# Performance work log

Measured on AMD Instinct MI355X. Metric: run time of the kernel, lower is better.

Reference implementation:

```python
import jax, jax.numpy as jnp
import numpy as np

B, T, D, H = 4, 2048, 1024, 16
HD = D // H  # head_dim = 64
SCALE = HD ** -0.5


def setup_inputs() -> dict:
    key = jax.random.key(0)
    k1, k2, k3 = jax.random.split(key, 3)
    x = jax.random.normal(k1, (B, T, D), dtype=jnp.float32)
    # xavier-uniform-like scaling for weights
    qkv_w = jax.random.normal(k2, (3 * D, D), dtype=jnp.float32) * (2.0 / (4 * D)) ** 0.5
    out_w = jax.random.normal(k3, (D, D), dtype=jnp.float32) * (1.0 / D) ** 0.5
    out_b = jnp.zeros((D,), dtype=jnp.float32)
    return {"x": x, "qkv_w": qkv_w, "out_w": out_w, "out_b": out_b}


def reference(x, qkv_w, out_w, out_b):
    Bx, Tx, _ = x.shape
    # qkv projection (nn.Linear: x @ W^T), no bias
    qkv = jnp.einsum('btd,ed->bte', x, qkv_w)  # [B,T,3D]
    qkv = qkv.reshape(Bx, Tx, 3, H, HD).transpose(2, 0, 3, 1, 4)  # [3,B,H,T,hd]
    q, k, v = qkv[0], qkv[1], qkv[2]
    scores = jnp.einsum('bhqd,bhkd->bhqk', q, k) * SCALE  # [B,H,T,T]
    causal = jnp.triu(jnp.ones((Tx, Tx), dtype=bool), k=1)
    scores = jnp.where(causal, -jnp.inf, scores)
    weights = jax.nn.softmax(scores, axis=-1)
    out = jnp.einsum('bhqk,bhkd->bhqd', weights, v)  # [B,H,T,hd]
    out = out.transpose(0, 2, 1, 3).reshape(Bx, Tx, D)
    return jnp.einsum('btd,ed->bte', out, out_w) + out_b
```

## Files before the change

### kernel.cpp

```cpp
#include <hip/hip_runtime.h>
#include <stdint.h>


typedef __bf16 bfx8 __attribute__((ext_vector_type(8)));
typedef float f32x4 __attribute__((ext_vector_type(4)));
typedef float f32x16 __attribute__((ext_vector_type(16)));

__device__ __forceinline__ uint16_t f2b(float f) {
  uint32_t u = __float_as_uint(f);
  u += 0x7fff + ((u >> 16) & 1);
  return (uint16_t)(u >> 16);
}

__device__ __forceinline__ uint32_t cvt_pk(float lo, float hi) {
  uint32_t r;
  asm("v_cvt_pk_bf16_f32 %0, %1, %2" : "=v"(r) : "v"(lo), "v"(hi));
  return r;
}

__device__ __forceinline__ void gld16(const void* g, void* l) {
  __builtin_amdgcn_global_load_lds((const __attribute__((address_space(1))) void*)g,
                                   (__attribute__((address_space(3))) void*)l,
                                   16, 0, 0);
}

__global__ __launch_bounds__(256) void cvt_all(const float* __restrict__ x,
                                               const float* __restrict__ w1,
                                               const float* __restrict__ w2,
                                               uint16_t* __restrict__ xb,
                                               uint16_t* __restrict__ w1b,
                                               uint16_t* __restrict__ w2b) {
  int i = blockIdx.x * 256 + threadIdx.x;
  const float* in;
  uint16_t* out;
  if (i < 1048576) { in = x; out = xb; }
  else if (i < 1048576 + 393216) { in = w1; out = w1b; i -= 1048576; }
  else { in = w2; out = w2b; i -= 1048576 + 393216; }
  float4 a = ((const float4*)in)[2 * i];
  float4 b = ((const float4*)in)[2 * i + 1];
  union { uint16_t u[8]; uint4 v; } pk;
  pk.u[0] = f2b(a.x); pk.u[1] = f2b(a.y); pk.u[2] = f2b(a.z); pk.u[3] = f2b(a.w);
  pk.u[4] = f2b(b.x); pk.u[5] = f2b(b.y); pk.u[6] = f2b(b.z); pk.u[7] = f2b(b.w);
  ((uint4*)out)[i] = pk.v;
}

template <int NI, int OUTF32, int QSC>
__global__ __launch_bounds__(512, 2) void gemm8p(const uint16_t* __restrict__ A,
                                                 const uint16_t* __restrict__ B,
                                                 void* __restrict__ Cout,
                                                 const float* __restrict__ bias,
                                                 int M, int N, int K, int nbx, int nwg) {
  constexpr int G0 = (NI + 1) / 2;
  constexpr int G1 = NI - G0;
  __shared__ alignas(16) uint16_t As[2][256 * 64];
  __shared__ alignas(16) uint16_t Bs[2][64 * NI * 64];

  int did = blockIdx.x;
  int wg = (did & 7) * (nwg >> 3) + (did >> 3);
  int bx = wg % nbx, by = wg / nbx;
  int m0 = by * 256, n0 = bx * (64 * NI);

  int tid = threadIdx.x, lane = tid & 63, wid = tid >> 6;
  int wm = wid >> 2, wn = wid & 3;
  int l15 = lane & 15;
  int ko = (lane >> 4) * 8;
  int sw = (l15 & 7) * 8;

  int srow = lane >> 3;
  int scol = ((lane & 7) ^ srow) * 8;

  f32x4 acc[8][NI] = {};

  auto stageA = [&](int buf, int t) {
    int k0 = t * 64;
#pragma unroll
    for (int i = 0; i < 4; ++i) {
      int r = wid * 32 + i * 8;
      gld16(&A[(size_t)(m0 + r + srow) * K + k0 + scol], &As[buf][r * 64]);
    }
  };
  auto stageB = [&](int buf, int t) {
    int k0 = t * 64;
#pragma unroll
    for (int i = 0; i < NI; ++i) {
      int r = wid * 8 * NI + i * 8;
      gld16(&B[(size_t)(n0 + r + srow) * K + k0 + scol], &Bs[buf][r * 64]);
    }
  };
  auto waitSteady = [&]() {
    if constexpr (NI == 3) asm volatile("s_waitcnt vmcnt(7)" ::: "memory");
    else                   asm volatile("s_waitcnt vmcnt(6)" ::: "memory");
  };

  stageA(0, 0); stageB(0, 0);
  stageA(1, 1); stageB(1, 1);
  waitSteady();
  __builtin_amdgcn_s_barrier();
  __builtin_amdgcn_sched_barrier(0);

  int nt = K >> 6;
  for (int t = 0; t < nt; ++t) {
    int buf = t & 1;
    const uint16_t* ap = &As[buf][0];
    const uint16_t* bp = &Bs[buf][0];
    bfx8 a[4][2], bg0[G0][2], bg1[G1][2], a2[4][2];

#pragma unroll
    for (int mi = 0; mi < 4; ++mi)
#pragma unroll
      for (int kk = 0; kk < 2; ++kk) {
        int r = wm * 128 + mi * 16 + l15;
        a[mi][kk] = *(const bfx8*)&ap[r * 64 + ((kk * 32 + ko) ^ sw)];
      }
#pragma unroll
    for (int ni = 0; ni < G0; ++ni)
#pragma unroll
      for (int kk = 0; kk < 2; ++kk) {
        int r = wn * (NI * 16) + ni * 16 + l15;
        bg0[ni][kk] = *(const bfx8*)&bp[r * 64 + ((kk * 32 + ko) ^ sw)];
      }
    __builtin_amdgcn_s_barrier();
    __builtin_amdgcn_s_setprio(1);
#pragma unroll
    for (int mi = 0; mi < 4; ++mi)
#pragma unroll
      for (int ni = 0; ni < G0; ++ni)
#pragma unroll
        for (int kk = 0; kk < 2; ++kk)
          acc[mi][ni] = __builtin_amdgcn_mfma_f32_16x16x32_bf16(a[mi][kk], bg0[ni][kk],
                                                                acc[mi][ni], 0, 0, 0);
    __builtin_amdgcn_s_setprio(0);
    __builtin_amdgcn_s_barrier();

#pragma unroll
    for (int ni = 0; ni < G1; ++ni)
#pragma unroll
      for (int kk = 0; kk < 2; ++kk) {
        int r = wn * (NI * 16) + (G0 + ni) * 16 + l15;
        bg1[ni][kk] = *(const bfx8*)&bp[r * 64 + ((kk * 32 + ko) ^ sw)];
      }
    __builtin_amdgcn_s_barrier();
    __builtin_amdgcn_s_setprio(1);
#pragma unroll
    for (int mi = 0; mi < 4; ++mi)
#pragma unroll
      for (int ni = 0; ni < G1; ++ni)
#pragma unroll
        for (int kk = 0; kk < 2; ++kk)
          acc[mi][G0 + ni] = __builtin_amdgcn_mfma_f32_16x16x32_bf16(a[mi][kk], bg1[ni][kk],
                                                                     acc[mi][G0 + ni], 0, 0, 0);
    __builtin_amdgcn_s_setprio(0);
    __builtin_amdgcn_s_barrier();

#pragma unroll
    for (int mi = 0; mi < 4; ++mi)
#pragma unroll
      for (int kk = 0; kk < 2; ++kk) {
        int r = wm * 128 + (mi + 4) * 16 + l15;
        a2[mi][kk] = *(const bfx8*)&ap[r * 64 + ((kk * 32 + ko) ^ sw)];
      }
    if (t + 2 < nt) stageB(buf, t + 2);
    __builtin_amdgcn_s_barrier();
    __builtin_amdgcn_s_setprio(1);
#pragma unroll
    for (int mi = 0; mi < 4; ++mi)
#pragma unroll
      for (int ni = 0; ni < G0; ++ni)
#pragma unroll
        for (int kk = 0; kk < 2; ++kk)
          acc[mi + 4][ni] = __builtin_amdgcn_mfma_f32_16x16x32_bf16(a2[mi][kk], bg0[ni][kk],
                                                                    acc[mi + 4][ni], 0, 0, 0);
    __builtin_amdgcn_s_setprio(0);
    __builtin_amdgcn_s_barrier();

    if (t + 2 < nt) {
      stageA(buf, t + 2);
      waitSteady();
    } else if (t + 2 == nt) {
      asm volatile("s_waitcnt vmcnt(0)" ::: "memory");
    }
    __builtin_amdgcn_sched_barrier(0);
    __builtin_amdgcn_s_barrier();
    __builtin_amdgcn_s_setprio(1);
#pragma unroll
    for (int mi = 0; mi < 4; ++mi)
#pragma unroll
      for (int ni = 0; ni < G1; ++ni)
#pragma unroll
        for (int kk = 0; kk < 2; ++kk)
          acc[mi + 4][G0 + ni] = __builtin_amdgcn_mfma_f32_16x16x32_bf16(a2[mi][kk], bg1[ni][kk],
                                                                         acc[mi + 4][G0 + ni], 0, 0, 0);
    __builtin_amdgcn_s_setprio(0);
    __builtin_amdgcn_s_barrier();
  }

#pragma unroll
  for (int mi = 0; mi < 8; ++mi) {
    int row = m0 + wm * 128 + mi * 16 + ((lane >> 4) << 2);
#pragma unroll
    for (int ni = 0; ni < NI; ++ni) {
      int col = n0 + wn * (NI * 16) + ni * 16 + l15;
      float qsc = (QSC && col < 1024) ? 0.18033688f : 1.0f;
#pragma unroll
      for (int r = 0; r < 4; ++r) {
        float v = acc[mi][ni][r];
        if (OUTF32)
          ((float*)Cout)[(size_t)(row + r) * N + col] = v + bias[col];
        else
          ((uint16_t*)Cout)[(size_t)(row + r) * N + col] = f2b(v * qsc);
      }
    }
  }
}

__global__ __launch_bounds__(256, 2) void flash_attn(const uint16_t* __restrict__ qkv,
                                                     uint16_t* __restrict__ attnb) {
  const int T = 2048, D3 = 3072;
  __shared__ alignas(16) uint16_t Ks[3][64 * 64];
  __shared__ alignas(16) uint16_t Vt[3][64 * 64];

  int d = blockIdx.x;
  int bh = d & 63;
  int a = d >> 6;
  int b = bh >> 4, h = bh & 15;

  int tid = threadIdx.x, lane = tid & 63, wid = tid >> 6;
  int l31 = lane & 31, hi = lane >> 5;
  int swz = (lane & 7) << 3;

  size_t base = (size_t)b * T * D3;
  int hoff = h * 64;
  const uint16_t* kbase = &qkv[base + 1024 + hoff];
  const uint16_t* vbase = &qkv[base + 2048 + hoff];

  int krow = wid * 16 + (lane >> 3);
  int kc = ((lane & 7) << 3) ^ ((krow & 7) << 3);
  int vr = (tid & 31) * 2;
  int vc = (tid >> 5) * 8;

  for (int p = 0; p < 2; ++p) {
    int qb = (p == 0) ? (15 - a) : a;
    int q0 = qb << 7;
    int qw = q0 + wid * 32;
    int ntile = 2 * qb + 2;

    float l_r = 0.f;
    f32x16 acc0 = {}, acc1 = {};
    bfx8 pf[4];
    int smax_prev = -1, vb_prev = 0;

    bfx8 qf[4];
    {
      const uint16_t* qp = &qkv[base + (size_t)(qw + l31) * D3 + hoff + 8 * hi];
#pragma unroll
      for (int h4 = 0; h4 < 4; ++h4) qf[h4] = *(const bfx8*)(qp + 16 * h4);
    }

    uint4 vA0, vA1, vB0, vB1;

    auto loadV = [&](int kv0, uint4& r0, uint4& r1) {
      r0 = *(const uint4*)&vbase[(size_t)(kv0 + vr) * D3 + vc];
      r1 = *(const uint4*)&vbase[(size_t)(kv0 + vr + 1) * D3 + vc];
    };
    auto stageK = [&](int buf, int kv0) {
      gld16(&kbase[(size_t)(kv0 + krow) * D3 + kc], &Ks[buf][wid * 1024]);
      gld16(&kbase[(size_t)(kv0 + krow + 8) * D3 + kc], &Ks[buf][wid * 1024 + 512]);
    };
    auto writeV = [&](int vb, const uint4& r0, const uint4& r1) {
      union { uint4 v; uint16_t u[8]; } x, y;
      x.v = r0; y.v = r1;
#pragma unroll
      for (int jj = 0; jj < 8; ++jj) {
        int hd = vc + jj;
        uint32_t pk = (uint32_t)x.u[jj] | ((uint32_t)y.u[jj] << 16);
        *(uint32_t*)&Vt[vb][hd * 64 + (vr ^ ((hd & 7) << 3))] = pk;
      }
    };
    auto doPV = [&]() {
      const uint16_t* vp = &Vt[vb_prev][0];
      __builtin_amdgcn_s_setprio(1);
#pragma unroll
      for (int s = 0; s < 4; ++s) {
        if (s <= smax_prev) {
          bfx8 v0 = *(const bfx8*)&vp[l31 * 64 + ((16 * s + 8 * hi) ^ swz)];
          acc0 = __builtin_amdgcn_mfma_f32_32x32x16_bf16(v0, pf[s], acc0, 0, 0, 0);
          bfx8 v1 = *(const bfx8*)&vp[(32 + l31) * 64 + ((16 * s + 8 * hi) ^ swz)];
          acc1 = __builtin_amdgcn_mfma_f32_32x32x16_bf16(v1, pf[s], acc1, 0, 0, 0);
        }
      }
      __builtin_amdgcn_s_setprio(0);
    };

    loadV(0, vA0, vA1);
    stageK(0, 0);
    writeV(0, vA0, vA1);
    loadV(64, vB0, vB1);
    stageK(1, 64);
    asm volatile("s_waitcnt vmcnt(0) lgkmcnt(0)" ::: "memory");
    __builtin_amdgcn_s_barrier();
    __builtin_amdgcn_sched_barrier(0);

    auto subiter = [&](int t, uint4& f0, uint4& f1, uint4& c0, uint4& c1) {
      int kv0 = t << 6;
      bool issue = (t + 2 < ntile);
      if (issue) {
        loadV((t + 2) << 6, f0, f1);
        stageK((t + 2) % 3, (t + 2) << 6);
      }
      bool active = (kv0 <= qw);
      int tmax = (qw > kv0) ? 2 : 1;
      f32x16 st0 = {}, st1 = {};
      if (active) {
        const uint16_t* kp = &Ks[t % 3][0];
        __builtin_amdgcn_s_setprio(1);
#pragma unroll
        for (int h4 = 0; h4 < 4; ++h4) {
          bfx8 kf0 = *(const bfx8*)&kp[l31 * 64 + ((16 * h4 + 8 * hi) ^ swz)];
          st0 = __builtin_amdgcn_mfma_f32_32x32x16_bf16(kf0, qf[h4], st0, 0, 0, 0);
          if (tmax == 2) {
            bfx8 kf1 = *(const bfx8*)&kp[(32 + l31) * 64 + ((16 * h4 + 8 * hi) ^ swz)];
            st1 = __builtin_amdgcn_mfma_f32_32x32x16_bf16(kf1, qf[h4], st1, 0, 0, 0);
          }
        }
        __builtin_amdgcn_s_setprio(0);
      }

      if (smax_prev >= 0) { doPV(); smax_prev = -1; }

      if (active) {
        int q = qw + l31;
        if (kv0 == qw) {
#pragma unroll
          for (int r = 0; r < 16; ++r) {
            int kv = kv0 + (r & 3) + 8 * (r >> 2) + 4 * hi;
            if (kv > q) st0[r] = -1e30f;
          }
        }
        if (tmax == 2 && kv0 + 32 == qw) {
#pragma unroll
          for (int r = 0; r < 16; ++r) {
            int kv = kv0 + 32 + (r & 3) + 8 * (r >> 2) + 4 * hi;
            if (kv > q) st1[r] = -1e30f;
          }
        }
        float l0 = 0.f, l1 = 0.f, l2 = 0.f, l3 = 0.f;
#pragma unroll
        for (int r = 0; r < 16; r += 4) {
          float e0 = __builtin_amdgcn_exp2f(st0[r]);
          float e1 = __builtin_amdgcn_exp2f(st0[r + 1]);
          float e2 = __builtin_amdgcn_exp2f(st0[r + 2]);
          float e3 = __builtin_amdgcn_exp2f(st0[r + 3]);
          st0[r] = e0; st0[r + 1] = e1; st0[r + 2] = e2; st0[r + 3] = e3;
          l0 += e0; l1 += e1; l2 += e2; l3 += e3;
        }
        if (tmax == 2) {
#pragma unroll
          for (int r = 0; r < 16; r += 4) {
            float e0 = __builtin_amdgcn_exp2f(st1[r]);
            float e1 = __builtin_amdgcn_exp2f(st1[r + 1]);
            float e2 = __builtin_amdgcn_exp2f(st1[r + 2]);
            float e3 = __builtin_amdgcn_exp2f(st1[r + 3]);
            st1[r] = e0; st1[r + 1] = e1; st1[r + 2] = e2; st1[r + 3] = e3;
            l0 += e0; l1 += e1; l2 += e2; l3 += e3;
          }
        }
        l_r += (l0 + l1) + (l2 + l3);

        int smax = (qw + 31 - kv0) >> 4;
        if (smax > 3) smax = 3;
#pragma unroll
        for (int s = 0; s < 4; ++s) {
          if (s <= smax) {
            int pb = 8 * (s & 1);
            uint32_t W0, W1, W2, W3;
            if (s < 2) {
              W0 = cvt_pk(st0[pb + 0], st0[pb + 1]);
              W1 = cvt_pk(st0[pb + 2], st0[pb + 3]);
              W2 = cvt_pk(st0[pb + 4], st0[pb + 5]);
              W3 = cvt_pk(st0[pb + 6], st0[pb + 7]);
            } else {
              W0 = cvt_pk(st1[pb + 0], st1[pb + 1]);
              W1 = cvt_pk(st1[pb + 2], st1[pb + 3]);
              W2 = cvt_pk(st1[pb + 4], st1[pb + 5]);
              W3 = cvt_pk(st1[pb + 6], st1[pb + 7]);
            }
            auto rA = __builtin_amdgcn_permlane32_swap(W0, W2, false, false);
            auto rB = __builtin_amdgcn_permlane32_swap(W1, W3, false, false);
            union { uint32_t u[4]; bfx8 v; } pk;
            pk.u[0] = rA[0]; pk.u[1] = rB[0]; pk.u[2] = rA[1]; pk.u[3] = rB[1];
            pf[s] = pk.v;
          }
        }
        smax_prev = smax;
        vb_prev = t % 3;
      }

      if (t + 1 < ntile) writeV((t + 1) % 3, c0, c1);

      if (issue)
        asm volatile("s_waitcnt vmcnt(4) lgkmcnt(0)" ::: "memory");
      else
        asm volatile("s_waitcnt vmcnt(0) lgkmcnt(0)" ::: "memory");
      __builtin_amdgcn_s_barrier();
      __builtin_amdgcn_sched_barrier(0);
    };

    for (int t = 0; t < ntile; t += 2) {
      subiter(t, vA0, vA1, vB0, vB1);
      subiter(t + 1, vB0, vB1, vA0, vA1);
    }
    if (smax_prev >= 0) doPV();

    float l_tot = l_r + __shfl_xor(l_r, 32);
    __syncthreads();
    uint16_t* ow = ((uint16_t*)Ks) + wid * 2048;
    float rl = 1.0f / l_tot;
#pragma unroll
    for (int f = 0; f < 2; ++f) {
#pragma unroll
      for (int r = 0; r < 16; r += 2) {
        int hd = 32 * f + (r & 3) + 8 * (r >> 2) + 4 * hi;
        float v0 = (f ? acc1[r] : acc0[r]) * rl;
        float v1 = (f ? acc1[r + 1] : acc0[r + 1]) * rl;
        *(uint32_t*)&ow[l31 * 64 + (hd ^ ((l31 & 7) << 3))] = cvt_pk(v0, v1);
      }
    }
    int row = lane >> 1, cb = (lane & 1) * 32;
    int q = q0 + wid * 32 + row;
    int rs = (row & 7) << 3;
    uint16_t* dst = &attnb[(size_t)(b * T + q) * 1024 + hoff + cb];
#pragma unroll
    for (int cc = 0; cc < 4; ++cc)
      *(uint4*)&dst[cc * 8] = *(const uint4*)&ow[row * 64 + ((cb + cc * 8) ^ rs)];
    __syncthreads();
  }
}

extern "C" void kernel_launch(void* const* d_in, const int* in_sizes, int n_in,
                              void* d_out, int out_size, void* d_ws, size_t ws_size,
                              hipStream_t stream) {
  const float* x = (const float*)d_in[0];
  const float* qkv_w = (const float*)d_in[1];
  const float* out_w = (const float*)d_in[2];
  const float* out_b = (const float*)d_in[3];
  float* out = (float*)d_out;

  char* ws = (char*)d_ws;
  uint16_t* xb    = (uint16_t*)(ws);
  uint16_t* qkvb  = (uint16_t*)(ws + 16777216);
  uint16_t* attnb = (uint16_t*)(ws + 67108864);
  uint16_t* wqkvb = (uint16_t*)(ws + 83886080);
  uint16_t* wob   = (uint16_t*)(ws + 90177536);

  cvt_all<<<6144, 256, 0, stream>>>(x, qkv_w, out_w, xb, wqkvb, wob);

  gemm8p<3, 0, 1><<<512, 512, 0, stream>>>(xb, wqkvb, (void*)qkvb, nullptr,
                                           8192, 3072, 1024, 16, 512);
  flash_attn<<<512, 256, 0, stream>>>(qkvb, attnb);
  gemm8p<2, 1, 0><<<256, 512, 0, stream>>>(attnb, wob, (void*)out, out_b,
                                           8192, 1024, 1024, 8, 256);
}
```

Baseline: 178.4 us.

## Widen flash-attention KV tile to 128 rows with double-buffered K

The flash attention loop now processes 128 KV rows per iteration instead of 64. That halves the iteration count and barriers and gives four 32-wide score tiles per step, with K double-buffered and V triple-buffered at the larger size. Global loads are now prefetched one tile ahead instead of two, and every iteration waits on vmcnt(0). This costs more LDS and registers (pf[8], st[4]) and exposes more load latency. It may also reduce occupancy and latency hiding.

Result: slower. 182.8 us (+2.4%).

```diff
diff --git a/kernel.cpp b/kernel.cpp
--- a/kernel.cpp
+++ b/kernel.cpp
@@ -216,8 +216,8 @@
 __global__ __launch_bounds__(256, 2) void flash_attn(const uint16_t* __restrict__ qkv,
                                                      uint16_t* __restrict__ attnb) {
   const int T = 2048, D3 = 3072;
-  __shared__ alignas(16) uint16_t Ks[3][64 * 64];
-  __shared__ alignas(16) uint16_t Vt[3][64 * 64];
+  __shared__ alignas(16) uint16_t Ks[2][128 * 64];
+  __shared__ alignas(16) uint16_t Vt[3][64 * 128];
 
   int d = blockIdx.x;
   int bh = d & 63;
@@ -233,20 +233,20 @@
   const uint16_t* kbase = &qkv[base + 1024 + hoff];
   const uint16_t* vbase = &qkv[base + 2048 + hoff];
 
-  int krow = wid * 16 + (lane >> 3);
-  int kc = ((lane & 7) << 3) ^ ((krow & 7) << 3);
-  int vr = (tid & 31) * 2;
+  int ksub = lane >> 3;
+  int kc = ((lane & 7) << 3) ^ (ksub << 3);
+  int vr4 = (tid & 31) * 4;
   int vc = (tid >> 5) * 8;
 
   for (int p = 0; p < 2; ++p) {
     int qb = (p == 0) ? (15 - a) : a;
     int q0 = qb << 7;
     int qw = q0 + wid * 32;
-    int ntile = 2 * qb + 2;
+    int ntile = qb + 1;
 
     float l_r = 0.f;
     f32x16 acc0 = {}, acc1 = {};
-    bfx8 pf[4];
+    bfx8 pf[8];
     int smax_prev = -1, vb_prev = 0;
 
     bfx8 qf[4];
@@ -256,70 +256,80 @@
       for (int h4 = 0; h4 < 4; ++h4) qf[h4] = *(const bfx8*)(qp + 16 * h4);
     }
 
-    uint4 vA0, vA1, vB0, vB1;
-
-    auto loadV = [&](int kv0, uint4& r0, uint4& r1) {
-      r0 = *(const uint4*)&vbase[(size_t)(kv0 + vr) * D3 + vc];
-      r1 = *(const uint4*)&vbase[(size_t)(kv0 + vr + 1) * D3 + vc];
+    uint4 v0r, v1r, v2r, v3r;
+
+    auto loadV = [&](int kv0) {
+      const uint16_t* vp = &vbase[(size_t)(kv0 + vr4) * D3 + vc];
+      v0r = *(const uint4*)vp;
+      v1r = *(const uint4*)(vp + D3);
+      v2r = *(const uint4*)(vp + 2 * D3);
+      v3r = *(const uint4*)(vp + 3 * D3);
     };
     auto stageK = [&](int buf, int kv0) {
-      gld16(&kbase[(size_t)(kv0 + krow) * D3 + kc], &Ks[buf][wid * 1024]);
-      gld16(&kbase[(size_t)(kv0 + krow + 8) * D3 + kc], &Ks[buf][wid * 1024 + 512]);
+#pragma unroll
+      for (int i = 0; i < 4; ++i) {
+        int r = wid * 32 + i * 8;
+        gld16(&kbase[(size_t)(kv0 + r + ksub) * D3 + kc], &Ks[buf][r * 64]);
+      }
     };
-    auto writeV = [&](int vb, const uint4& r0, const uint4& r1) {
-      union { uint4 v; uint16_t u[8]; } x, y;
-      x.v = r0; y.v = r1;
-#pragma unroll
-      for (int jj = 0; jj < 8; ++jj) {
-        int hd = vc + jj;
-        uint32_t pk = (uint32_t)x.u[jj] | ((uint32_t)y.u[jj] << 16);
-        *(uint32_t*)&Vt[vb][hd * 64 + (vr ^ ((hd & 7) << 3))] = pk;
+    auto writeV = [&](int vb) {
+      union { uint4 v; uint16_t u[8]; } x0, x1, x2, x3;
+      x0.v = v0r; x1.v = v1r; x2.v = v2r; x3.v = v3r;
+#pragma unroll
+      for (int j = 0; j < 8; ++j) {
+        int hd = vc + j;
+        uint2 val;
+        val.x = (uint32_t)x0.u[j] | ((uint32_t)x1.u[j] << 16);
+        val.y = (uint32_t)x2.u[j] | ((uint32_t)x3.u[j] << 16);
+        *(uint2*)&Vt[vb][hd * 128 + (vr4 ^ ((hd & 7) << 3))] = val;
       }
     };
     auto doPV = [&]() {
       const uint16_t* vp = &Vt[vb_prev][0];
       __builtin_amdgcn_s_setprio(1);
 #pragma unroll
-      for (int s = 0; s < 4; ++s) {
+      for (int s = 0; s < 8; ++s) {
         if (s <= smax_prev) {
-          bfx8 v0 = *(const bfx8*)&vp[l31 * 64 + ((16 * s + 8 * hi) ^ swz)];
-          acc0 = __builtin_amdgcn_mfma_f32_32x32x16_bf16(v0, pf[s], acc0, 0, 0, 0);
-          bfx8 v1 = *(const bfx8*)&vp[(32 + l31) * 64 + ((16 * s + 8 * hi) ^ swz)];
-          acc1 = __builtin_amdgcn_mfma_f32_32x32x16_bf16(v1, pf[s], acc1, 0, 0, 0);
+          bfx8 va = *(const bfx8*)&vp[l31 * 128 + ((16 * s + 8 * hi) ^ swz)];
+          acc0 = __builtin_amdgcn_mfma_f32_32x32x16_bf16(va, pf[s], acc0, 0, 0, 0);
+          bfx8 vb2 = *(const bfx8*)&vp[(32 + l31) * 128 + ((16 * s + 8 * hi) ^ swz)];
+          acc1 = __builtin_amdgcn_mfma_f32_32x32x16_bf16(vb2, pf[s], acc1, 0, 0, 0);
         }
       }
       __builtin_amdgcn_s_setprio(0);
     };
 
-    loadV(0, vA0, vA1);
+    loadV(0);
     stageK(0, 0);
-    writeV(0, vA0, vA1);
-    loadV(64, vB0, vB1);
-    stageK(1, 64);
+    writeV(0);
     asm volatile("s_waitcnt vmcnt(0) lgkmcnt(0)" ::: "memory");
     __builtin_amdgcn_s_barrier();
     __builtin_amdgcn_sched_barrier(0);
 
-    auto subiter = [&](int t, uint4& f0, uint4& f1, uint4& c0, uint4& c1) {
-      int kv0 = t << 6;
-      bool issue = (t + 2 < ntile);
+    for (int t = 0; t < ntile; ++t) {
+      int kv0 = t << 7;
+      bool issue = (t + 1 < ntile);
       if (issue) {
-        loadV((t + 2) << 6, f0, f1);
-        stageK((t + 2) % 3, (t + 2) << 6);
+        loadV((t + 1) << 7);
+        stageK((t + 1) & 1, (t + 1) << 7);
       }
       bool active = (kv0 <= qw);
-      int tmax = (qw > kv0) ? 2 : 1;
-      f32x16 st0 = {}, st1 = {};
+      int dq = qw - kv0;
+      int tmax = 4, sd = -1;
+      if (active && dq < 128) { tmax = (dq >> 5) + 1; sd = dq >> 5; }
+      f32x16 st[4] = {};
+
       if (active) {
-        const uint16_t* kp = &Ks[t % 3][0];
+        const uint16_t* kp = &Ks[t & 1][0];
         __builtin_amdgcn_s_setprio(1);
 #pragma unroll
         for (int h4 = 0; h4 < 4; ++h4) {
-          bfx8 kf0 = *(const bfx8*)&kp[l31 * 64 + ((16 * h4 + 8 * hi) ^ swz)];
-          st0 = __builtin_amdgcn_mfma_f32_32x32x16_bf16(kf0, qf[h4], st0, 0, 0, 0);
-          if (tmax == 2) {
-            bfx8 kf1 = *(const bfx8*)&kp[(32 + l31) * 64 + ((16 * h4 + 8 * hi) ^ swz)];
-            st1 = __builtin_amdgcn_mfma_f32_32x32x16_bf16(kf1, qf[h4], st1, 0, 0, 0);
+#pragma unroll
+          for (int s = 0; s < 4; ++s) {
+            if (s < tmax) {
+              bfx8 kf = *(const bfx8*)&kp[(32 * s + l31) * 64 + ((16 * h4 + 8 * hi) ^ swz)];
+              st[s] = __builtin_amdgcn_mfma_f32_32x32x16_bf16(kf, qf[h4], st[s], 0, 0, 0);
+            }
           }
         }
         __builtin_amdgcn_s_setprio(0);
@@ -329,85 +339,60 @@
 
       if (active) {
         int q = qw + l31;
-        if (kv0 == qw) {
-#pragma unroll
-          for (int r = 0; r < 16; ++r) {
-            int kv = kv0 + (r & 3) + 8 * (r >> 2) + 4 * hi;
-            if (kv > q) st0[r] = -1e30f;
-          }
-        }
-        if (tmax == 2 && kv0 + 32 == qw) {
-#pragma unroll
-          for (int r = 0; r < 16; ++r) {
-            int kv = kv0 + 32 + (r & 3) + 8 * (r >> 2) + 4 * hi;
-            if (kv > q) st1[r] = -1e30f;
+#pragma unroll
+        for (int s = 0; s < 4; ++s) {
+          if (s == sd) {
+#pragma unroll
+            for (int r = 0; r < 16; ++r) {
+              int kv = kv0 + 32 * s + (r & 3) + 8 * (r >> 2) + 4 * hi;
+              if (kv > q) st[s][r] = -1e30f;
+            }
           }
         }
         float l0 = 0.f, l1 = 0.f, l2 = 0.f, l3 = 0.f;
 #pragma unroll
-        for (int r = 0; r < 16; r += 4) {
-          float e0 = __builtin_amdgcn_exp2f(st0[r]);
-          float e1 = __builtin_amdgcn_exp2f(st0[r + 1]);
-          float e2 = __builtin_amdgcn_exp2f(st0[r + 2]);
-          float e3 = __builtin_amdgcn_exp2f(st0[r + 3]);
-          st0[r] = e0; st0[r + 1] = e1; st0[r + 2] = e2; st0[r + 3] = e3;
-          l0 += e0; l1 += e1; l2 += e2; l3 += e3;
-        }
-        if (tmax == 2) {
-#pragma unroll
-          for (int r = 0; r < 16; r += 4) {
-            float e0 = __builtin_amdgcn_exp2f(st1[r]);
-            float e1 = __builtin_amdgcn_exp2f(st1[r + 1]);
-            float e2 = __builtin_amdgcn_exp2f(st1[r + 2]);
-            float e3 = __builtin_amdgcn_exp2f(st1[r + 3]);
-            st1[r] = e0; st1[r + 1] = e1; st1[r + 2] = e2; st1[r + 3] = e3;
-            l0 += e0; l1 += e1; l2 += e2; l3 += e3;
+        for (int s = 0; s < 4; ++s) {
+          if (s < tmax) {
+#pragma unroll
+            for (int r = 0; r < 16; r += 4) {
+              float e0 = __builtin_amdgcn_exp2f(st[s][r]);
+              float e1 = __builtin_amdgcn_exp2f(st[s][r + 1]);
+              float e2 = __builtin_amdgcn_exp2f(st[s][r + 2]);
+              float e3 = __builtin_amdgcn_exp2f(st[s][r + 3]);
+              st[s][r] = e0; st[s][r + 1] = e1; st[s][r + 2] = e2; st[s][r + 3] = e3;
+              l0 += e0; l1 += e1; l2 += e2; l3 += e3;
+            }
           }
         }
         l_r += (l0 + l1) + (l2 + l3);
 
-        int smax = (qw + 31 - kv0) >> 4;
-        if (smax > 3) smax = 3;
-#pragma unroll
-        for (int s = 0; s < 4; ++s) {
-          if (s <= smax) {
-            int pb = 8 * (s & 1);
-            uint32_t W0, W1, W2, W3;
-            if (s < 2) {
-              W0 = cvt_pk(st0[pb + 0], st0[pb + 1]);
-              W1 = cvt_pk(st0[pb + 2], st0[pb + 3]);
-              W2 = cvt_pk(st0[pb + 4], st0[pb + 5]);
-              W3 = cvt_pk(st0[pb + 6], st0[pb + 7]);
-            } else {
-              W0 = cvt_pk(st1[pb + 0], st1[pb + 1]);
-              W1 = cvt_pk(st1[pb + 2], st1[pb + 3]);
-              W2 = cvt_pk(st1[pb + 4], st1[pb + 5]);
-              W3 = cvt_pk(st1[pb + 6], st1[pb + 7]);
-            }
+        int smax = (dq + 31) >> 4;
+        if (smax > 7) smax = 7;
+#pragma unroll
+        for (int s8 = 0; s8 < 8; ++s8) {
+          if (s8 <= smax) {
+            int pb = 8 * (s8 & 1);
+            const f32x16& src = st[s8 >> 1];
+            uint32_t W0 = cvt_pk(src[pb + 0], src[pb + 1]);
+            uint32_t W1 = cvt_pk(src[pb + 2], src[pb + 3]);
+            uint32_t W2 = cvt_pk(src[pb + 4], src[pb + 5]);
+            uint32_t W3 = cvt_pk(src[pb + 6], src[pb + 7]);
             auto rA = __builtin_amdgcn_permlane32_swap(W0, W2, false, false);
             auto rB = __builtin_amdgcn_permlane32_swap(W1, W3, false, false);
             union { uint32_t u[4]; bfx8 v; } pk;
             pk.u[0] = rA[0]; pk.u[1] = rB[0]; pk.u[2] = rA[1]; pk.u[3] = rB[1];
-            pf[s] = pk.v;
+            pf[s8] = pk.v;
           }
         }
         smax_prev = smax;
         vb_prev = t % 3;
       }
 
-      if (t + 1 < ntile) writeV((t + 1) % 3, c0, c1);
-
-      if (issue)
-        asm volatile("s_waitcnt vmcnt(4) lgkmcnt(0)" ::: "memory");
-      else
-        asm volatile("s_waitcnt vmcnt(0) lgkmcnt(0)" ::: "memory");
+      if (issue) writeV((t + 1) % 3);
+
+      asm volatile("s_waitcnt vmcnt(0) lgkmcnt(0)" ::: "memory");
       __builtin_amdgcn_s_barrier();
       __builtin_amdgcn_sched_barrier(0);
-    };
-
-    for (int t = 0; t < ntile; t += 2) {
-      subiter(t, vA0, vA1, vB0, vB1);
-      subiter(t + 1, vB0, vB1, vA0, vA1);
     }
     if (smax_prev >= 0) doPV();
 
```

## Split causal attention KV range across two blocks and merge partials

Applied to the files above, without the earlier changes.

The attention kernel now launches twice as many blocks. Each block processes two KV segments for two different query blocks and writes unnormalized bf16 partial outputs plus row sums into reused workspace buffers. A new merge kernel adds the two partials and divides by the combined row sum. The KV prefetch pipeline drops from three-deep to two-deep with a full wait every iteration. The aim is more parallelism, paid for with an extra pass over memory, a second bf16 rounding and less load/compute overlap.

Result: slower. 196.8 us (+10.3%).

```diff
diff --git a/kernel.cpp b/kernel.cpp
--- a/kernel.cpp
+++ b/kernel.cpp
@@ -214,14 +214,16 @@
 }
 
 __global__ __launch_bounds__(256, 2) void flash_attn(const uint16_t* __restrict__ qkv,
-                                                     uint16_t* __restrict__ attnb) {
+                                                     uint16_t* __restrict__ pb0,
+                                                     uint16_t* __restrict__ pb1,
+                                                     float* __restrict__ lbuf) {
   const int T = 2048, D3 = 3072;
-  __shared__ alignas(16) uint16_t Ks[3][64 * 64];
+  __shared__ alignas(16) uint16_t Ks[2][64 * 64];
   __shared__ alignas(16) uint16_t Vt[3][64 * 64];
 
   int d = blockIdx.x;
   int bh = d & 63;
-  int a = d >> 6;
+  int j = d >> 6;
   int b = bh >> 4, h = bh & 15;
 
   int tid = threadIdx.x, lane = tid & 63, wid = tid >> 6;
@@ -238,11 +240,13 @@
   int vr = (tid & 31) * 2;
   int vc = (tid >> 5) * 8;
 
-  for (int p = 0; p < 2; ++p) {
-    int qb = (p == 0) ? (15 - a) : a;
+  for (int seg = 0; seg < 2; ++seg) {
+    int qb   = (seg == 0) ? (15 - j) : j;
+    int t0   = (seg == 0) ? 0 : (j + 1);
+    int tend = (seg == 0) ? (16 - j) : (2 * j + 2);
+    uint16_t* pbuf = (seg == 0) ? pb0 : pb1;
     int q0 = qb << 7;
     int qw = q0 + wid * 32;
-    int ntile = 2 * qb + 2;
 
     float l_r = 0.f;
     f32x16 acc0 = {}, acc1 = {};
@@ -256,19 +260,19 @@
       for (int h4 = 0; h4 < 4; ++h4) qf[h4] = *(const bfx8*)(qp + 16 * h4);
     }
 
-    uint4 vA0, vA1, vB0, vB1;
-
-    auto loadV = [&](int kv0, uint4& r0, uint4& r1) {
-      r0 = *(const uint4*)&vbase[(size_t)(kv0 + vr) * D3 + vc];
-      r1 = *(const uint4*)&vbase[(size_t)(kv0 + vr + 1) * D3 + vc];
+    uint4 v0r, v1r;
+
+    auto loadV = [&](int kv0) {
+      v0r = *(const uint4*)&vbase[(size_t)(kv0 + vr) * D3 + vc];
+      v1r = *(const uint4*)&vbase[(size_t)(kv0 + vr + 1) * D3 + vc];
     };
     auto stageK = [&](int buf, int kv0) {
       gld16(&kbase[(size_t)(kv0 + krow) * D3 + kc], &Ks[buf][wid * 1024]);
       gld16(&kbase[(size_t)(kv0 + krow + 8) * D3 + kc], &Ks[buf][wid * 1024 + 512]);
     };
-    auto writeV = [&](int vb, const uint4& r0, const uint4& r1) {
+    auto writeV = [&](int vb) {
       union { uint4 v; uint16_t u[8]; } x, y;
-      x.v = r0; y.v = r1;
+      x.v = v0r; y.v = v1r;
 #pragma unroll
       for (int jj = 0; jj < 8; ++jj) {
         int hd = vc + jj;
@@ -282,36 +286,35 @@
 #pragma unroll
       for (int s = 0; s < 4; ++s) {
         if (s <= smax_prev) {
-          bfx8 v0 = *(const bfx8*)&vp[l31 * 64 + ((16 * s + 8 * hi) ^ swz)];
-          acc0 = __builtin_amdgcn_mfma_f32_32x32x16_bf16(v0, pf[s], acc0, 0, 0, 0);
-          bfx8 v1 = *(const bfx8*)&vp[(32 + l31) * 64 + ((16 * s + 8 * hi) ^ swz)];
-          acc1 = __builtin_amdgcn_mfma_f32_32x32x16_bf16(v1, pf[s], acc1, 0, 0, 0);
+          bfx8 va = *(const bfx8*)&vp[l31 * 64 + ((16 * s + 8 * hi) ^ swz)];
+          acc0 = __builtin_amdgcn_mfma_f32_32x32x16_bf16(va, pf[s], acc0, 0, 0, 0);
+          bfx8 vb2 = *(const bfx8*)&vp[(32 + l31) * 64 + ((16 * s + 8 * hi) ^ swz)];
+          acc1 = __builtin_amdgcn_mfma_f32_32x32x16_bf16(vb2, pf[s], acc1, 0, 0, 0);
         }
       }
       __builtin_amdgcn_s_setprio(0);
     };
 
-    loadV(0, vA0, vA1);
-    stageK(0, 0);
-    writeV(0, vA0, vA1);
-    loadV(64, vB0, vB1);
-    stageK(1, 64);
+    stageK(t0 & 1, t0 << 6);
+    loadV(t0 << 6);
     asm volatile("s_waitcnt vmcnt(0) lgkmcnt(0)" ::: "memory");
+    writeV(t0 % 3);
+    asm volatile("s_waitcnt lgkmcnt(0)" ::: "memory");
     __builtin_amdgcn_s_barrier();
     __builtin_amdgcn_sched_barrier(0);
 
-    auto subiter = [&](int t, uint4& f0, uint4& f1, uint4& c0, uint4& c1) {
+    for (int t = t0; t < tend; ++t) {
       int kv0 = t << 6;
-      bool issue = (t + 2 < ntile);
+      bool issue = (t + 1 < tend);
       if (issue) {
-        loadV((t + 2) << 6, f0, f1);
-        stageK((t + 2) % 3, (t + 2) << 6);
+        stageK((t + 1) & 1, (t + 1) << 6);
+        loadV((t + 1) << 6);
       }
       bool active = (kv0 <= qw);
       int tmax = (qw > kv0) ? 2 : 1;
       f32x16 st0 = {}, st1 = {};
       if (active) {
-        const uint16_t* kp = &Ks[t % 3][0];
+        const uint16_t* kp = &Ks[t & 1][0];
         __builtin_amdgcn_s_setprio(1);
 #pragma unroll
         for (int h4 = 0; h4 < 4; ++h4) {
@@ -395,45 +398,61 @@
         vb_prev = t % 3;
       }
 
-      if (t + 1 < ntile) writeV((t + 1) % 3, c0, c1);
-
-      if (issue)
-        asm volatile("s_waitcnt vmcnt(4) lgkmcnt(0)" ::: "memory");
-      else
-        asm volatile("s_waitcnt vmcnt(0) lgkmcnt(0)" ::: "memory");
+      if (issue) writeV((t + 1) % 3);
+
+      asm volatile("s_waitcnt vmcnt(0) lgkmcnt(0)" ::: "memory");
       __builtin_amdgcn_s_barrier();
       __builtin_amdgcn_sched_barrier(0);
-    };
-
-    for (int t = 0; t < ntile; t += 2) {
-      subiter(t, vA0, vA1, vB0, vB1);
-      subiter(t + 1, vB0, vB1, vA0, vA1);
     }
     if (smax_prev >= 0) doPV();
 
     float l_tot = l_r + __shfl_xor(l_r, 32);
     __syncthreads();
     uint16_t* ow = ((uint16_t*)Ks) + wid * 2048;
-    float rl = 1.0f / l_tot;
 #pragma unroll
     for (int f = 0; f < 2; ++f) {
 #pragma unroll
       for (int r = 0; r < 16; r += 2) {
         int hd = 32 * f + (r & 3) + 8 * (r >> 2) + 4 * hi;
-        float v0 = (f ? acc1[r] : acc0[r]) * rl;
-        float v1 = (f ? acc1[r + 1] : acc0[r + 1]) * rl;
+        float v0 = (f ? acc1[r] : acc0[r]);
+        float v1 = (f ? acc1[r + 1] : acc0[r + 1]);
         *(uint32_t*)&ow[l31 * 64 + (hd ^ ((l31 & 7) << 3))] = cvt_pk(v0, v1);
       }
     }
     int row = lane >> 1, cb = (lane & 1) * 32;
     int q = q0 + wid * 32 + row;
     int rs = (row & 7) << 3;
-    uint16_t* dst = &attnb[(size_t)(b * T + q) * 1024 + hoff + cb];
+    uint16_t* dst = &pbuf[(size_t)(b * T + q) * 1024 + hoff + cb];
 #pragma unroll
     for (int cc = 0; cc < 4; ++cc)
       *(uint4*)&dst[cc * 8] = *(const uint4*)&ow[row * 64 + ((cb + cc * 8) ^ rs)];
+    if (lane < 32)
+      lbuf[seg * 131072 + bh * 2048 + qw + l31] = l_tot;
     __syncthreads();
   }
+}
+
+__global__ __launch_bounds__(256) void merge_attn(const uint16_t* __restrict__ pA,
+                                                  uint16_t* __restrict__ pBout,
+                                                  const float* __restrict__ lbuf) {
+  int i = blockIdx.x * 256 + threadIdx.x;
+  int row = i >> 7;
+  int c8 = (i & 127) << 3;
+  int q = row & 2047, b = row >> 11;
+  int h = c8 >> 6;
+  int lidx = ((b << 4) + h) * 2048 + q;
+  float r = 1.0f / (lbuf[lidx] + lbuf[131072 + lidx]);
+  size_t off = (size_t)row * 1024 + c8;
+  union { uint4 v; uint16_t u[8]; } a, bb, o;
+  a.v = *(const uint4*)&pA[off];
+  bb.v = *(const uint4*)&pBout[off];
+#pragma unroll
+  for (int k = 0; k < 8; ++k) {
+    float fa = __uint_as_float((uint32_t)a.u[k] << 16);
+    float fb = __uint_as_float((uint32_t)bb.u[k] << 16);
+    o.u[k] = f2b((fa + fb) * r);
+  }
+  *(uint4*)&pBout[off] = o.v;
 }
 
 extern "C" void kernel_launch(void* const* d_in, const int* in_sizes, int n_in,
@@ -456,7 +475,8 @@
 
   gemm8p<3, 0, 1><<<512, 512, 0, stream>>>(xb, wqkvb, (void*)qkvb, nullptr,
                                            8192, 3072, 1024, 16, 512);
-  flash_attn<<<512, 256, 0, stream>>>(qkvb, attnb);
+  flash_attn<<<1024, 256, 0, stream>>>(qkvb, xb, attnb, (float*)wqkvb);
+  merge_attn<<<4096, 256, 0, stream>>>(xb, attnb, (const float*)wqkvb);
   gemm8p<2, 1, 0><<<256, 512, 0, stream>>>(attnb, wob, (void*)out, out_b,
                                            8192, 1024, 1024, 8, 256);
 }
```
